# Performance work log

Hardware: AMD Instinct MI355X
Metric: run time of the kernel (lower is better)

The kernel has to match this reference:

```python
import jax, jax.numpy as jnp
import numpy as np

NEG = jnp.float32(-1e30)  # finite stand-in for -inf (keeps grads NaN-free)

B, S = 8, 256


def _inside_logZ(scores, mask):
    """CYK inside algorithm. scores/mask: [B, S, S]. Returns scalar logZ.

    Recurrence (widths w = 1..S-1, processed as a scan over anti-diagonals):
      s[i, i+1] = scores[i, i+1]
      s[i, i+w] = scores[i, i+w] + logsumexp_{k=i+1..i+w-1} (s[i, k] + s[k, i+w])
    logZ = sum_b s[b, 0, lens[b]].
    """
    Bsz, Sl, _ = scores.shape
    lens = mask[:, 0].sum(-1)                    # [B] sentence lengths
    idx = jnp.arange(Sl)
    rows = idx[:, None]                          # [S,1] span start i
    m = idx[None, :]                             # [1,S] split offset (k = i+m)
    km = jnp.clip(rows + m, 0, Sl - 1)           # [S,S] split index k, clipped reads

    def step(s, w):
        # s: [B,S,S] chart. Process all spans of width w at once.
        j = jnp.clip(rows + w, 0, Sl - 1)        # [S,1] span end (clipped)
        left = s[:, rows, km]                    # s[b, i, i+m]      -> [B,S,S]
        right = s[:, km, j]                      # s[b, i+m, i+w]    -> [B,S,S]
        valid = (m >= 1) & (m <= w - 1) & (rows + w < Sl)
        lse = jax.nn.logsumexp(jnp.where(valid, left + right, NEG), axis=-1)  # [B,S]
        diag = scores[:, idx, jnp.clip(idx + w, 0, Sl - 1)]                    # [B,S]
        val = diag + jnp.where(w == 1, 0.0, lse)
        # scatter onto the w-th diagonal; out-of-range (i+w >= S) lanes dropped
        s = s.at[:, idx, idx + w].set(val, mode='drop')
        return s, None

    s0 = jnp.full((Bsz, Sl, Sl), NEG, scores.dtype)
    s, _ = jax.lax.scan(step, s0, jnp.arange(1, Sl))
    return s[jnp.arange(Bsz), 0, lens].sum()


def setup_inputs() -> dict:
    key = jax.random.key(0)
    scores = jax.random.normal(key, (B, S, S), dtype=jnp.float32)
    # strict upper-triangular mask (all sentences full length S-1 tokens)
    mask = jnp.triu(jnp.ones((S, S), dtype=bool), k=1)
    mask = jnp.broadcast_to(mask, (B, S, S))
    return {"scores": scores, "mask": mask}


def reference(scores, mask):
    # forward(scores, mask, target=None, mbr=True): marginals = d logZ / d scores
    marginals = jax.grad(lambda sc: _inside_logZ(sc, mask))(scores)
    return marginals
```

## Files before the change

kernel.cpp:

```cpp
#include <hip/hip_runtime.h>

#define SL 256
#define BATCH 8
#define NT 1024
#define W0 16
#define LDSF 33152
#define TABN 264
#define LDSB ((LDSF + 32 + TABN + 3 * 256) * 4)

__device__ __forceinline__ int rowOff(int j) {
  int jp = (j > 128) ? (256 - j) : j;
  int base = (jp - 1) * 260;
  if (j > 128) base += (jp + 3) & ~3;
  return base;
}

template <int G>
__device__ __forceinline__ float grpSum(float v) {
#pragma unroll
  for (int o = G >> 1; o; o >>= 1) v += __shfl_xor(v, o, 64);
  return v;
}

__device__ __forceinline__ void barrier_lgkm() {
  __builtin_amdgcn_sched_barrier(0);
  asm volatile("s_waitcnt lgkmcnt(0)" ::: "memory");
  __builtin_amdgcn_s_barrier();
  __builtin_amdgcn_sched_barrier(0);
}

__device__ void rescaleE(int tid, float dc, int wcur, float* sh,
                         float* Es1, float* Es2, float* Es3,
                         const int* __restrict__ tab) {
  const int lane = tid & 63, wave = tid >> 6;
  for (int j = 1 + wave; j < SL; j += 16) {
    int jlo = j - wcur; if (jlo < 0) jlo = 0;
    int base = tab[j];
    for (int i = jlo + lane; i < j; i += 64)
      sh[base + i] *= __expf(-dc * (float)(j - i));
  }
  const float f1 = __expf(-dc);
  const float f2 = f1 * f1;
  const float f3 = f2 * f1;
  for (int x = tid; x < SL; x += NT) {
    Es1[x] *= f1; Es2[x] *= f2; Es3[x] *= f3;
  }
}

template <int G>
__device__ void insideP(int wlo, int whi, int t0, int tid,
                        const float* __restrict__ sc, float* __restrict__ sh,
                        float* __restrict__ red, const int* __restrict__ tab,
                        float* __restrict__ Es1, float* __restrict__ Es2,
                        float* __restrict__ Es3) {
  constexpr int LG = (G == 4) ? 2 : (G == 8) ? 3 : (G == 16) ? 4 : 5;
  constexpr int NG = 64 / G;
  const int lane = tid & 63, wv = tid >> 6;
  const int l = lane >> LG, lig = lane & (G - 1);
  const int i = wv * (NG - 1) + l;
  for (int w = wlo; w <= whi; w += 2) {
    const int t = t0 + ((w - wlo) >> 1);
    const float fl = red[16 + ((t - 1) & 1)];
    const unsigned wm1 = (unsigned)(w - 1);
    const unsigned wm2 = (unsigned)(w - 2);
    const bool vw = i < SL - w;
    const bool vw1 = (l < NG - 1) && (i < SL - w - 1);
    const int jw = (i + w < SL) ? i + w : SL - 1;
    const int jw1 = (i + w + 1 < SL) ? i + w + 1 : SL - 1;
    const int ojw = tab[jw], ojw1 = tab[jw1];
    const float scw = sc[i * SL + jw];
    const float scw1 = sc[i * SL + jw1];
    float a0 = 0.f, a1 = 0.f, b0 = 0.f, b1 = 0.f;
    if (vw) {
      for (int s4 = ((i + 1) & ~3) + 4 * lig; s4 < i + w; s4 += 4 * G) {
        float4 rw = *(const float4*)(sh + ojw + s4);
        float4 rw1 = *(const float4*)(sh + ojw1 + s4);
        int4 tv = *(const int4*)(tab + s4);
        float e0 = sh[tv.x + i], e1 = sh[tv.y + i];
        float e2 = sh[tv.z + i], e3 = sh[tv.w + i];
        const int d0 = s4 - i;
        float f0 = ((unsigned)(d0 - 1) < wm1) ? e0 : 0.f;
        float f1 = ((unsigned)(d0    ) < wm1) ? e1 : 0.f;
        float f2 = ((unsigned)(d0 + 1) < wm1) ? e2 : 0.f;
        float f3 = ((unsigned)(d0 + 2) < wm1) ? e3 : 0.f;
        a0 = fmaf(f0, rw.x, a0); a1 = fmaf(f1, rw.y, a1);
        a0 = fmaf(f2, rw.z, a0); a1 = fmaf(f3, rw.w, a1);
        float g0 = ((unsigned)(d0 - 2) < wm2) ? e0 : 0.f;
        float g1 = ((unsigned)(d0 - 1) < wm2) ? e1 : 0.f;
        float g2 = ((unsigned)(d0    ) < wm2) ? e2 : 0.f;
        float g3 = ((unsigned)(d0 + 1) < wm2) ? e3 : 0.f;
        b0 = fmaf(g0, rw1.x, b0); b1 = fmaf(g1, rw1.y, b1);
        b0 = fmaf(g2, rw1.z, b0); b1 = fmaf(g3, rw1.w, b1);
      }
    }
    float accw = grpSum<G>(a0 + a1);
    float accw1 = grpSum<G>(b0 + b1);
    float Ew = __expf(scw) * accw;
    if (vw && lig == 0) {
      sh[ojw + i] = Ew;
      if (accw > 3.5e19f || accw < 3e-16f) red[16 + (t & 1)] = fmaxf(accw, 1e-30f);
    }
    float EwN = __shfl_down(Ew, G, 64);
    if (vw1) {
      float tot = accw1 + Es1[i] * EwN + Ew * Es1[jw];
      if (lig == 0) {
        sh[ojw1 + i] = __expf(scw1) * tot;
        if (tot > 3.5e19f || tot < 3e-16f) red[16 + (t & 1)] = fmaxf(tot, 1e-30f);
      }
    }
    __syncthreads();
    if (fl != 0.f) {
      float dc = (__logf(fl) + 8.0f) / (float)(w - 2);
      rescaleE(tid, dc, w + 1, sh, Es1, Es2, Es3, tab);
      __syncthreads();
      if (tid == 0) { red[16] = 0.f; red[17] = 0.f; }
      __syncthreads();
    }
  }
}

template <int G>
__device__ void insideQ(int wlo, int whi, int t0, int tid,
                        const float* __restrict__ sc, float* __restrict__ sh,
                        float* __restrict__ red, const int* __restrict__ tab,
                        float* __restrict__ Es1, float* __restrict__ Es2,
                        float* __restrict__ Es3) {
  constexpr int LG = (G == 4) ? 2 : 3;
  constexpr int NG = 64 / G;
  const int lane = tid & 63, wv = tid >> 6;
  const int l = lane >> LG, lig = lane & (G - 1);
  const int i = wv * (NG - 3) + l;
  for (int w = wlo; w <= whi; w += 4) {
    const int t = t0 + ((w - wlo) >> 2);
    const float fl = red[16 + ((t - 1) & 1)];
    const bool v0 = i < SL - w;
    const bool v1 = i < SL - w - 1;
    const bool v2 = i < SL - w - 2;
    const bool v3 = i < SL - w - 3;
    const int j0 = (i + w < SL) ? i + w : SL - 1;
    const int j1 = (i + w + 1 < SL) ? i + w + 1 : SL - 1;
    const int j2 = (i + w + 2 < SL) ? i + w + 2 : SL - 1;
    const int j3 = (i + w + 3 < SL) ? i + w + 3 : SL - 1;
    const int o0 = tab[j0], o1 = tab[j1], o2 = tab[j2], o3 = tab[j3];
    const int rb = i * SL;
    const float s0 = sc[rb + j0], s1 = sc[rb + j1];
    const float s2 = sc[rb + j2], s3 = sc[rb + j3];
    float a0=0.f,a1=0.f,b0=0.f,b1=0.f,c0=0.f,c1=0.f,e4a=0.f,e4b=0.f;
    if (v0) {
      const unsigned mA = (unsigned)(w - 1);
      const unsigned mB = (unsigned)(w - 2);
      const unsigned mC = (unsigned)(w - 3);
      const unsigned mD = (unsigned)(w - 4);
      for (int s4 = ((i + 1) & ~3) + 4 * lig; s4 < i + w; s4 += 4 * G) {
        float4 r0 = *(const float4*)(sh + o0 + s4);
        float4 r1 = *(const float4*)(sh + o1 + s4);
        float4 r2 = *(const float4*)(sh + o2 + s4);
        float4 r3 = *(const float4*)(sh + o3 + s4);
        int4 tv = *(const int4*)(tab + s4);
        float e0 = sh[tv.x + i], e1 = sh[tv.y + i];
        float e2 = sh[tv.z + i], e3 = sh[tv.w + i];
        const int dd = s4 - i;
        float f0 = ((unsigned)(dd - 1) < mA) ? e0 : 0.f;
        float f1 = ((unsigned)(dd    ) < mA) ? e1 : 0.f;
        float f2 = ((unsigned)(dd + 1) < mA) ? e2 : 0.f;
        float f3 = ((unsigned)(dd + 2) < mA) ? e3 : 0.f;
        a0 = fmaf(f0, r0.x, a0); a1 = fmaf(f1, r0.y, a1);
        a0 = fmaf(f2, r0.z, a0); a1 = fmaf(f3, r0.w, a1);
        float g0 = ((unsigned)(dd - 2) < mB) ? e0 : 0.f;
        float g1 = ((unsigned)(dd - 1) < mB) ? e1 : 0.f;
        float g2 = ((unsigned)(dd    ) < mB) ? e2 : 0.f;
        float g3 = ((unsigned)(dd + 1) < mB) ? e3 : 0.f;
        b0 = fmaf(g0, r1.x, b0); b1 = fmaf(g1, r1.y, b1);
        b0 = fmaf(g2, r1.z, b0); b1 = fmaf(g3, r1.w, b1);
        float h0 = ((unsigned)(dd - 3) < mC) ? e0 : 0.f;
        float h1 = ((unsigned)(dd - 2) < mC) ? e1 : 0.f;
        float h2 = ((unsigned)(dd - 1) < mC) ? e2 : 0.f;
        float h3 = ((unsigned)(dd    ) < mC) ? e3 : 0.f;
        c0 = fmaf(h0, r2.x, c0); c1 = fmaf(h1, r2.y, c1);
        c0 = fmaf(h2, r2.z, c0); c1 = fmaf(h3, r2.w, c1);
        float k0 = ((unsigned)(dd - 4) < mD) ? e0 : 0.f;
        float k1 = ((unsigned)(dd - 3) < mD) ? e1 : 0.f;
        float k2 = ((unsigned)(dd - 2) < mD) ? e2 : 0.f;
        float k3 = ((unsigned)(dd - 1) < mD) ? e3 : 0.f;
        e4a = fmaf(k0, r3.x, e4a); e4b = fmaf(k1, r3.y, e4b);
        e4a = fmaf(k2, r3.z, e4a); e4b = fmaf(k3, r3.w, e4b);
      }
    }
    float A0 = grpSum<G>(a0 + a1);
    float A1 = grpSum<G>(b0 + b1);
    float A2 = grpSum<G>(c0 + c1);
    float A3 = grpSum<G>(e4a + e4b);
    const float es1i = Es1[i], es2i = Es2[i], es3i = Es3[i];
    const float E0 = __expf(s0) * A0;
    const float n10 = __shfl_down(E0, G, 64);
    const float n20 = __shfl_down(E0, 2 * G, 64);
    const float n30 = __shfl_down(E0, 3 * G, 64);
    const float T1 = A1 + es1i * n10 + E0 * Es1[j0];
    const float E1v = __expf(s1) * T1;
    const float n11 = __shfl_down(E1v, G, 64);
    const float n21 = __shfl_down(E1v, 2 * G, 64);
    const float T2 = A2 + es1i * n11 + E1v * Es1[j1] + es2i * n20 + E0 * Es2[j0];
    const float E2v = __expf(s2) * T2;
    const float n12 = __shfl_down(E2v, G, 64);
    const float T3 = A3 + es1i * n12 + E2v * Es1[j2] + es2i * n21 + E1v * Es2[j1]
                        + es3i * n30 + E0 * Es3[j0];
    const float E3v = __expf(s3) * T3;
    if (lig == 0) {
      if (v0)                sh[o0 + i] = E0;
      if (v1 && l <= NG - 2) sh[o1 + i] = E1v;
      if (v2 && l <= NG - 3) sh[o2 + i] = E2v;
      if (v3 && l <= NG - 4) sh[o3 + i] = E3v;
      if (v0 && (A0 > 3.5e19f || A0 < 3e-16f)) red[16 + (t & 1)] = fmaxf(A0, 1e-30f);
      if (v3 && l <= NG - 4 && (T3 > 3.5e19f || T3 < 3e-16f))
        red[16 + (t & 1)] = fmaxf(T3, 1e-30f);
    }
    __syncthreads();
    if (fl != 0.f) {
      float dc = (__logf(fl) + 8.0f) / (float)(w - 3);
      rescaleE(tid, dc, w + 3, sh, Es1, Es2, Es3, tab);
      __syncthreads();
      if (tid == 0) { red[16] = 0.f; red[17] = 0.f; }
      __syncthreads();
    }
  }
}

template <int G>
__device__ void outsideP(int wAhi, int wAlo, int tid, const float* __restrict__ sc,
                         float* __restrict__ gOut, const float* __restrict__ Eg,
                         const float* __restrict__ ETg, float* __restrict__ shH,
                         const int* __restrict__ tab, const float* __restrict__ Es1) {
  constexpr int LG = (G == 4) ? 2 : (G == 8) ? 3 : (G == 16) ? 4 : 5;
  constexpr int NG = 64 / G;
  const int lane = tid & 63, wv = tid >> 6;
  const int l = lane >> LG, lig = lane & (G - 1);
  const int p = wv * (NG - 1) + l;
  for (int wA = wAhi; wA >= wAlo; wA -= 2) {
    const int wB = wA - 1;
    const bool vA = p < SL - wA;
    const bool vB = (l >= 1 || wv == 0) && (p < SL - wB);
    const int qA = p + wA, qB = p + wB;
    const int qAc = (qA < SL) ? qA : SL - 1;
    const int qBc = (qB < SL) ? qB : SL - 1;
    const int oA = tab[qAc], oB = tab[qBc];
    const float scA = sc[p * SL + qAc];
    const float scB = sc[p * SL + qBc];
    float EpA = 0.f, EpB = 0.f;
    if (lig == 0) {
      if (vA) EpA = Eg[p * SL + qA];
      if (vB) EpB = Eg[p * SL + qB];
    }
    float a0 = 0.f, a1 = 0.f, b0 = 0.f, b1 = 0.f;
    if (vA || vB) {
      const float* erA = Eg + (size_t)qAc * SL;
      const float* erB = Eg + (size_t)qBc * SL;
      for (int s4 = ((qA + 1) & ~3) + 4 * lig; s4 < SL; s4 += 4 * G) {
        float4 eA = *(const float4*)(erA + s4);
        float4 eB = *(const float4*)(erB + s4);
        int4 tv = *(const int4*)(tab + s4);
        float h0 = shH[tv.x + p], h1 = shH[tv.y + p];
        float h2 = shH[tv.z + p], h3 = shH[tv.w + p];
        float m0 = (s4 + 0 > qA) ? h0 : 0.f, m1 = (s4 + 1 > qA) ? h1 : 0.f;
        float m2 = (s4 + 2 > qA) ? h2 : 0.f, m3 = (s4 + 3 > qA) ? h3 : 0.f;
        a0 = fmaf(eA.x, m0, a0); a1 = fmaf(eA.y, m1, a1);
        a0 = fmaf(eA.z, m2, a0); a1 = fmaf(eA.w, m3, a1);
        b0 = fmaf(eB.x, m0, b0); b1 = fmaf(eB.y, m1, b1);
        b0 = fmaf(eB.z, m2, b0); b1 = fmaf(eB.w, m3, b1);
      }
      for (int s4 = 4 * lig; s4 < p; s4 += 4 * G) {
        float4 ev = *(const float4*)(ETg + (size_t)p * SL + s4);
        float4 hA = *(const float4*)(shH + oA + s4);
        float4 hB = *(const float4*)(shH + oB + s4);
        a0 = fmaf(ev.x, hA.x, a0); a1 = fmaf(ev.y, hA.y, a1);
        a0 = fmaf(ev.z, hA.z, a0); a1 = fmaf(ev.w, hA.w, a1);
        float n0 = (s4 + 0 < p - 1) ? hB.x : 0.f;
        float n1 = (s4 + 1 < p - 1) ? hB.y : 0.f;
        float n2 = (s4 + 2 < p - 1) ? hB.z : 0.f;
        float n3 = (s4 + 3 < p - 1) ? hB.w : 0.f;
        b0 = fmaf(ev.x, n0, b0); b1 = fmaf(ev.y, n1, b1);
        b0 = fmaf(ev.z, n2, b0); b1 = fmaf(ev.w, n3, b1);
      }
    }
    float accA = grpSum<G>(a0 + a1);
    float accBb = grpSum<G>(b0 + b1);
    float HA = __expf(scA) * accA;
    if (vA && lig == 0) {
      shH[oA + p] = HA;
      gOut[p * SL + qA] = EpA * accA;
    }
    float HAup = __shfl_up(HA, G, 64);
    if (vB) {
      float accB = accBb + (vA ? Es1[qBc] * HA : 0.f)
                         + ((p > 0) ? Es1[p - 1] * HAup : 0.f);
      if (lig == 0) {
        shH[oB + p] = __expf(scB) * accB;
        gOut[p * SL + qB] = EpB * accB;
      }
    }
    barrier_lgkm();
  }
}

template <int G>
__device__ void outsideQ(int wAhi, int wAlo, int tid, const float* __restrict__ sc,
                         float* __restrict__ gOut, const float* __restrict__ Eg,
                         const float* __restrict__ ETg, float* __restrict__ shH,
                         const int* __restrict__ tab, const float* __restrict__ Es1,
                         const float* __restrict__ Es2, const float* __restrict__ Es3) {
  constexpr int LG = (G == 4) ? 2 : 3;
  constexpr int NG = 64 / G;
  const int lane = tid & 63, wv = tid >> 6;
  const int l = lane >> LG, lig = lane & (G - 1);
  const int p = wv * (NG - 3) + l;
  for (int wA = wAhi; wA >= wAlo; wA -= 4) {
    const bool v0 = p < SL - wA;
    const bool v1 = p < SL - wA + 1;
    const bool v2 = p < SL - wA + 2;
    const bool v3 = p < SL - wA + 3;
    const int q0 = p + wA, q1 = q0 - 1, q2 = q0 - 2, q3 = q0 - 3;
    const int qc0 = (q0 < SL) ? q0 : SL - 1;
    const int qc1 = (q1 < SL) ? q1 : SL - 1;
    const int qc2 = (q2 < SL) ? q2 : SL - 1;
    const int qc3 = (q3 < SL) ? q3 : SL - 1;
    const int o0 = tab[qc0], o1 = tab[qc1], o2 = tab[qc2], o3 = tab[qc3];
    const int rb = p * SL;
    const float s0 = sc[rb + qc0], s1 = sc[rb + qc1];
    const float s2 = sc[rb + qc2], s3 = sc[rb + qc3];
    float Ep0 = 0.f, Ep1 = 0.f, Ep2 = 0.f, Ep3 = 0.f;
    if (lig == 0) {
      if (v0) Ep0 = Eg[rb + q0];
      if (v1) Ep1 = Eg[rb + q1];
      if (v2) Ep2 = Eg[rb + q2];
      if (v3) Ep3 = Eg[rb + q3];
    }
    float a0=0.f,a1=0.f,b0=0.f,b1=0.f,c0=0.f,c1=0.f,e4a=0.f,e4b=0.f;
    if (v3) {
      const float* er0 = Eg + (size_t)qc0 * SL;
      const float* er1 = Eg + (size_t)qc1 * SL;
      const float* er2 = Eg + (size_t)qc2 * SL;
      const float* er3 = Eg + (size_t)qc3 * SL;
      for (int s4 = ((q0 + 1) & ~3) + 4 * lig; s4 < SL; s4 += 4 * G) {
        float4 e0v = *(const float4*)(er0 + s4);
        float4 e1v = *(const float4*)(er1 + s4);
        float4 e2v = *(const float4*)(er2 + s4);
        float4 e3v = *(const float4*)(er3 + s4);
        int4 tv = *(const int4*)(tab + s4);
        float h0 = (s4 + 0 > q0) ? shH[tv.x + p] : 0.f;
        float h1 = (s4 + 1 > q0) ? shH[tv.y + p] : 0.f;
        float h2 = (s4 + 2 > q0) ? shH[tv.z + p] : 0.f;
        float h3 = (s4 + 3 > q0) ? shH[tv.w + p] : 0.f;
        a0 = fmaf(e0v.x, h0, a0); a1 = fmaf(e0v.y, h1, a1);
        a0 = fmaf(e0v.z, h2, a0); a1 = fmaf(e0v.w, h3, a1);
        b0 = fmaf(e1v.x, h0, b0); b1 = fmaf(e1v.y, h1, b1);
        b0 = fmaf(e1v.z, h2, b0); b1 = fmaf(e1v.w, h3, b1);
        c0 = fmaf(e2v.x, h0, c0); c1 = fmaf(e2v.y, h1, c1);
        c0 = fmaf(e2v.z, h2, c0); c1 = fmaf(e2v.w, h3, c1);
        e4a = fmaf(e3v.x, h0, e4a); e4b = fmaf(e3v.y, h1, e4b);
        e4a = fmaf(e3v.z, h2, e4a); e4b = fmaf(e3v.w, h3, e4b);
      }
      for (int s4 = 4 * lig; s4 < p; s4 += 4 * G) {
        float4 ev = *(const float4*)(ETg + (size_t)p * SL + s4);
        float4 h0v = *(const float4*)(shH + o0 + s4);
        float4 h1v = *(const float4*)(shH + o1 + s4);
        float4 h2v = *(const float4*)(shH + o2 + s4);
        float4 h3v = *(const float4*)(shH + o3 + s4);
        a0 = fmaf(ev.x, h0v.x, a0); a1 = fmaf(ev.y, h0v.y, a1);
        a0 = fmaf(ev.z, h0v.z, a0); a1 = fmaf(ev.w, h0v.w, a1);
        float n0 = (s4 + 0 < p - 1) ? h1v.x : 0.f;
        float n1 = (s4 + 1 < p - 1) ? h1v.y : 0.f;
        float n2 = (s4 + 2 < p - 1) ? h1v.z : 0.f;
        float n3 = (s4 + 3 < p - 1) ? h1v.w : 0.f;
        b0 = fmaf(ev.x, n0, b0); b1 = fmaf(ev.y, n1, b1);
        b0 = fmaf(ev.z, n2, b0); b1 = fmaf(ev.w, n3, b1);
        float x0 = (s4 + 0 < p - 2) ? h2v.x : 0.f;
        float x1 = (s4 + 1 < p - 2) ? h2v.y : 0.f;
        float x2 = (s4 + 2 < p - 2) ? h2v.z : 0.f;
        float x3 = (s4 + 3 < p - 2) ? h2v.w : 0.f;
        c0 = fmaf(ev.x, x0, c0); c1 = fmaf(ev.y, x1, c1);
        c0 = fmaf(ev.z, x2, c0); c1 = fmaf(ev.w, x3, c1);
        float y0 = (s4 + 0 < p - 3) ? h3v.x : 0.f;
        float y1 = (s4 + 1 < p - 3) ? h3v.y : 0.f;
        float y2 = (s4 + 2 < p - 3) ? h3v.z : 0.f;
        float y3 = (s4 + 3 < p - 3) ? h3v.w : 0.f;
        e4a = fmaf(ev.x, y0, e4a); e4b = fmaf(ev.y, y1, e4b);
        e4a = fmaf(ev.z, y2, e4a); e4b = fmaf(ev.w, y3, e4b);
      }
    }
    float A0 = grpSum<G>(a0 + a1);
    float A1 = grpSum<G>(b0 + b1);
    float A2 = grpSum<G>(c0 + c1);
    float A3 = grpSum<G>(e4a + e4b);
    const float ep1 = (p >= 1) ? Es1[p - 1] : 0.f;
    const float ep2 = (p >= 2) ? Es2[p - 2] : 0.f;
    const float ep3 = (p >= 3) ? Es3[p - 3] : 0.f;
    const float H0 = __expf(s0) * A0;
    const float u10 = __shfl_up(H0, G, 64);
    const float u20 = __shfl_up(H0, 2 * G, 64);
    const float u30 = __shfl_up(H0, 3 * G, 64);
    const float T1 = A1 + (v0 ? Es1[qc1] * H0 : 0.f) + ep1 * u10;
    const float H1 = __expf(s1) * T1;
    const float u11 = __shfl_up(H1, G, 64);
    const float u21 = __shfl_up(H1, 2 * G, 64);
    const float T2 = A2 + (v1 ? Es1[qc2] * H1 : 0.f) + ep1 * u11
                        + (v0 ? Es2[qc2] * H0 : 0.f) + ep2 * u20;
    const float H2 = __expf(s2) * T2;
    const float u12 = __shfl_up(H2, G, 64);
    const float T3 = A3 + (v2 ? Es1[qc3] * H2 : 0.f) + ep1 * u12
                        + (v1 ? Es2[qc3] * H1 : 0.f) + ep2 * u21
                        + (v0 ? Es3[qc3] * H0 : 0.f) + ep3 * u30;
    const float H3 = __expf(s3) * T3;
    const bool okl1 = (l >= 1) || (wv == 0);
    const bool okl2 = (l >= 2) || (wv == 0);
    const bool okl3 = (l >= 3) || (wv == 0);
    if (lig == 0) {
      if (v0)         { shH[o0 + p] = H0; gOut[rb + q0] = Ep0 * A0; }
      if (v1 && okl1) { shH[o1 + p] = H1; gOut[rb + q1] = Ep1 * T1; }
      if (v2 && okl2) { shH[o2 + p] = H2; gOut[rb + q2] = Ep2 * T2; }
      if (v3 && okl3) { shH[o3 + p] = H3; gOut[rb + q3] = Ep3 * T3; }
    }
    barrier_lgkm();
  }
}

template <int G>
__device__ void outsideB(int w0, int w1, int tid,
    const float* __restrict__ sc, float* __restrict__ gOut,
    const float* __restrict__ Eg, const float* __restrict__ ETg,
    float* __restrict__ shH, const int* __restrict__ tab) {
  constexpr int LG = (G == 4) ? 2 : (G == 8) ? 3 : (G == 16) ? 4 : (G == 32) ? 5 : 6;
  const int c = tid >> LG, lig = tid & (G - 1);
  for (int w = w0; w >= w1; --w) {
    if (c < SL - w) {
      const int p = c, q = p + w;
      float scv = 0.f, Epq = 0.f;
      if (lig == 0) { scv = sc[p * SL + q]; Epq = Eg[p * SL + q]; }
      float a0 = 0.f, a1 = 0.f;
      const float* er = Eg + (size_t)q * SL;
      for (int s4 = ((q + 1) & ~3) + 4 * lig; s4 < SL; s4 += 4 * G) {
        float4 ev = *(const float4*)(er + s4);
        int4 tv = *(const int4*)(tab + s4);
        float h0 = shH[tv.x + p], h1 = shH[tv.y + p];
        float h2 = shH[tv.z + p], h3 = shH[tv.w + p];
        a0 = fmaf(ev.x, (s4 + 0 > q) ? h0 : 0.f, a0);
        a1 = fmaf(ev.y, (s4 + 1 > q) ? h1 : 0.f, a1);
        a0 = fmaf(ev.z, (s4 + 2 > q) ? h2 : 0.f, a0);
        a1 = fmaf(ev.w, (s4 + 3 > q) ? h3 : 0.f, a1);
      }
      if (p > 0) {
        const float* et = ETg + (size_t)p * SL;
        const float* hq = shH + tab[q];
        for (int s4 = 4 * lig; s4 < p; s4 += 4 * G) {
          float4 ev = *(const float4*)(et + s4);
          float4 hv = *(const float4*)(hq + s4);
          a0 = fmaf(ev.x, hv.x, a0);
          a1 = fmaf(ev.y, hv.y, a1);
          a0 = fmaf(ev.z, hv.z, a0);
          a1 = fmaf(ev.w, hv.w, a1);
        }
      }
      float acc = grpSum<G>(a0 + a1);
      if (lig == 0) {
        gOut[p * SL + q] = Epq * acc;
        shH[tab[q] + p] = acc * __expf(scv);
      }
    }
    barrier_lgkm();
  }
}

__global__ __launch_bounds__(NT) void cyk_quad(
    const float* __restrict__ scores, float* __restrict__ out,
    float* __restrict__ ws) {
  extern __shared__ float sh[];
  float* red = sh + LDSF;
  int* tab = (int*)(sh + LDSF + 32);
  float* Es1 = sh + LDSF + 32 + TABN;
  float* Es2 = Es1 + 256;
  float* Es3 = Es2 + 256;
  const int b = blockIdx.x;
  const int tid = threadIdx.x;
  const int lane = tid & 63;
  const int wave = tid >> 6;
  const size_t P = (size_t)SL * SL;
  const float* sc = scores + (size_t)b * P;
  float* g   = out + (size_t)b * P;
  float* Eg  = ws + (size_t)b * P;
  float* ETg = ws + (size_t)(BATCH + b) * P;

  for (int idx = tid * 4; idx < LDSF; idx += NT * 4)
    *(float4*)(sh + idx) = make_float4(0.f, 0.f, 0.f, 0.f);
  if (tid < 32) red[tid] = 0.f;
  if (tid < TABN) tab[tid] = (tid >= 1 && tid <= 255) ? rowOff(tid) : 0;
  if (tid < 256) { Es1[tid] = 0.f; Es2[tid] = 0.f; Es3[tid] = 0.f; }
  __syncthreads();

  for (int i = tid; i < SL - 1; i += NT)
    sh[tab[i + 1] + i] = sc[i * SL + i + 1];
  __syncthreads();

  {
    const int c4 = tid >> 2, lig = tid & 3;
    for (int w = 2; w <= W0; ++w) {
      if (c4 < SL - w) {
        const int i = c4, j = i + w;
        const int oj = tab[j];
        float scv = 0.f;
        if (lig == 0) scv = sc[i * SL + j];
        float m = -1e30f, sum = 0.f;
        for (int k = i + 1 + lig; k < j; k += 4) {
          float t = sh[tab[k] + i] + sh[oj + k];
          float nm = fmaxf(m, t);
          sum = sum * __expf(m - nm) + __expf(t - nm);
          m = nm;
        }
#pragma unroll
        for (int o = 2; o; o >>= 1) {
          float mo = __shfl_xor(m, o, 64);
          float so = __shfl_xor(sum, o, 64);
          float nm = fmaxf(m, mo);
          sum = sum * __expf(m - nm) + so * __expf(mo - nm);
          m = nm;
        }
        if (lig == 0) sh[oj + i] = scv + m + __logf(sum);
      }
      __syncthreads();
    }
  }

  {
    int idx = tid < SL - W0 ? tid : SL - W0 - 1;
    float v = sh[tab[idx + W0] + idx];
#pragma unroll
    for (int o = 32; o; o >>= 1) v = fmaxf(v, __shfl_xor(v, o, 64));
    if (lane == 0) red[wave] = v;
  }
  __syncthreads();
  float cc;
  {
    float mx = red[0];
#pragma unroll
    for (int t = 1; t < 16; ++t) mx = fmaxf(mx, red[t]);
    cc = mx / (float)W0;
  }

  for (int w = 1; w <= W0; ++w) {
    for (int i = tid; i < SL - w; i += NT) {
      int o = tab[i + w] + i;
      float E = __expf(sh[o] - cc * (float)w);
      sh[o] = E;
      if (w == 1) Es1[i] = E;
      if (w == 2) Es2[i] = E;
      if (w == 3) Es3[i] = E;
    }
  }
  if (tid == 0) { red[16] = 0.f; red[17] = 0.f; }
  __syncthreads();

  insideP<4>(17, 43, 1, tid, sc, sh, red, tab, Es1, Es2, Es3);
  insideQ<4>(45, 169, 15, tid, sc, sh, red, tab, Es1, Es2, Es3);
  insideQ<8>(173, 249, 47, tid, sc, sh, red, tab, Es1, Es2, Es3);
  insideP<32>(253, 253, 67, tid, sc, sh, red, tab, Es1, Es2, Es3);

  {
    float acc = 0.f;
    if (wave == 0) {
      const int o255 = tab[255];
      for (int k = 1 + lane; k < 255; k += 64)
        acc += sh[tab[k]] * sh[o255 + k];
#pragma unroll
      for (int o = 32; o; o >>= 1) acc += __shfl_xor(acc, o, 64);
      if (lane == 0) sh[o255] = __expf(sc[SL - 1]) * acc;
    }
    __syncthreads();
  }

  for (int idx = tid; idx < SL * SL; idx += NT) {
    int j = idx >> 8, i = idx & 255;
    if (i < j) ETg[idx] = sh[tab[j] + i];
  }
  for (int idx = tid; idx < SL * SL; idx += NT) {
    int i = idx >> 8, k = idx & 255;
    if (k > i) Eg[idx] = sh[tab[k] + i];
  }
  if (tid == 0) {
    float Er = sh[tab[SL - 1]];
    red[20] = (Er > 0.f) ? __expf(sc[SL - 1]) / Er : 0.f;
    g[SL - 1] = 1.0f;
  }
  __syncthreads();

  for (int idx = tid * 4; idx < LDSF; idx += NT * 4)
    *(float4*)(sh + idx) = make_float4(0.f, 0.f, 0.f, 0.f);
  __syncthreads();
  if (tid == 0) sh[tab[SL - 1]] = red[20];
  __syncthreads();

  outsideP<32>(254, 254, tid, sc, g, Eg, ETg, sh, tab, Es1);
  outsideQ<8>(252, 176, tid, sc, g, Eg, ETg, sh, tab, Es1, Es2, Es3);
  outsideQ<4>(172, 48, tid, sc, g, Eg, ETg, sh, tab, Es1, Es2, Es3);
  outsideP<4>(44, 18, tid, sc, g, Eg, ETg, sh, tab, Es1);
  outsideB<4>(16, 1, tid, sc, g, Eg, ETg, sh, tab);
}

__device__ __forceinline__ float grpMaxR(float v, int G) {
#pragma unroll
  for (int o = 32; o; o >>= 1)
    if (o < G) v = fmaxf(v, __shfl_xor(v, o, 64));
  return v;
}
__device__ __forceinline__ float grpSumR(float v, int G) {
#pragma unroll
  for (int o = 32; o; o >>= 1)
    if (o < G) v += __shfl_xor(v, o, 64);
  return v;
}

__global__ __launch_bounds__(NT) void cyk_io_fb(
    const float* __restrict__ scores, float* __restrict__ out,
    float* __restrict__ ws) {
  const int b = blockIdx.x;
  const int tid = threadIdx.x;
  const size_t P = (size_t)SL * SL;
  const float* sc = scores + (size_t)b * P;
  float* g = out + (size_t)b * P;
  float* s = ws + (size_t)b * P;
  float* l = ws + (size_t)(BATCH + b) * P;

  for (int i = tid; i < SL - 1; i += NT) {
    s[i * SL + i + 1] = sc[i * SL + i + 1];
    l[i * SL + i + 1] = 0.f;
  }
  __syncthreads();

  for (int w = 2; w < SL; ++w) {
    const int cells = SL - w;
    int G = NT / cells;
    G = (G >= 64) ? 64 : (1 << (31 - __clz(G)));
    const int lg = 31 - __clz(G);
    const int c = tid >> lg;
    const int lig = tid & (G - 1);
    if (c < cells) {
      const int i = c, j = i + w;
      const float* srow = s + i * SL;
      float m = -INFINITY;
      for (int k = i + 1 + lig; k < j; k += G)
        m = fmaxf(m, srow[k] + s[k * SL + j]);
      m = grpMaxR(m, G);
      float sum = 0.f;
      for (int k = i + 1 + lig; k < j; k += G)
        sum += __expf(srow[k] + s[k * SL + j] - m);
      sum = grpSumR(sum, G);
      if (lig == 0) {
        const float lse = m + __logf(sum);
        s[i * SL + j] = sc[i * SL + j] + lse;
        l[i * SL + j] = lse;
      }
    }
    __syncthreads();
  }

  if (tid == 0) g[0 * SL + (SL - 1)] = 1.0f;
  __syncthreads();

  for (int w = SL - 2; w >= 1; --w) {
    const int cells = SL - w;
    int G = NT / cells;
    G = (G >= 64) ? 64 : (1 << (31 - __clz(G)));
    const int lg = 31 - __clz(G);
    const int c = tid >> lg;
    const int lig = tid & (G - 1);
    if (c < cells) {
      const int p = c, q = p + w;
      const float spq = s[p * SL + q];
      const int TR = SL - 1 - q;
      const int T = TR + p;
      float acc = 0.f;
      for (int t = lig; t < T; t += G) {
        if (t < TR) {
          const int j = q + 1 + t;
          acc += g[p * SL + j] * __expf(spq + s[q * SL + j] - l[p * SL + j]);
        } else {
          const int i = t - TR;
          acc += g[i * SL + q] * __expf(s[i * SL + p] + spq - l[i * SL + q]);
        }
      }
      acc = grpSumR(acc, G);
      if (lig == 0) g[p * SL + q] = acc;
    }
    __syncthreads();
  }
}

extern "C" void kernel_launch(void* const* d_in, const int* in_sizes, int n_in,
                              void* d_out, int out_size, void* d_ws, size_t ws_size,
                              hipStream_t stream) {
  const float* scores = (const float*)d_in[0];
  float* out = (float*)d_out;
  float* ws = (float*)d_ws;

  const size_t sq = (size_t)SL * SL * sizeof(float);
  hipMemsetAsync(d_out, 0, (size_t)BATCH * sq, stream);

  int dev = 0;
  hipGetDevice(&dev);
  int maxShm = 0;
  hipDeviceGetAttribute(&maxShm, hipDeviceAttributeMaxSharedMemoryPerBlock, dev);
  (void)hipFuncSetAttribute(reinterpret_cast<const void*>(cyk_quad),
                            hipFuncAttributeMaxDynamicSharedMemorySize, LDSB);

  if (maxShm >= LDSB && ws_size >= (size_t)2 * BATCH * sq) {
    hipMemsetAsync(ws, 0, (size_t)2 * BATCH * sq, stream);
    cyk_quad<<<BATCH, NT, LDSB, stream>>>(scores, out, ws);
  } else {
    cyk_io_fb<<<BATCH, NT, 0, stream>>>(scores, out, ws);
  }
}
```

Baseline: 653.7 us.

## Mirror inside/outside chart rows in global memory for contiguous float4 operand loads

Each inside and outside value is now also written to a row-major global copy (Eg, plus a new Hg buffer), so the inner split loops read one operand as a contiguous float4 from global memory. This replaces four table-indexed scalar LDS gathers per chunk. The inner loops are also split into an unmasked steady-state body with masked head and tail chunks, and the end-of-inside Eg copy loop is dropped. In exchange, rescaling must now sweep the whole global Eg array, the workspace grows to three buffers that must be zeroed, and the outside barrier changes from barrier_lgkm to __syncthreads so that global writes become visible; each step's operands now depend on global memory latency and coherence within the block.

```diff
diff --git a/kernel.cpp b/kernel.cpp
--- a/kernel.cpp
+++ b/kernel.cpp
@@ -31,7 +31,7 @@
 
 __device__ void rescaleE(int tid, float dc, int wcur, float* sh,
                          float* Es1, float* Es2, float* Es3,
-                         const int* __restrict__ tab) {
+                         const int* __restrict__ tab, float* __restrict__ Eg) {
   const int lane = tid & 63, wave = tid >> 6;
   for (int j = 1 + wave; j < SL; j += 16) {
     int jlo = j - wcur; if (jlo < 0) jlo = 0;
@@ -39,6 +39,11 @@
     for (int i = jlo + lane; i < j; i += 64)
       sh[base + i] *= __expf(-dc * (float)(j - i));
   }
+  for (int idx = tid; idx < SL * SL; idx += NT) {
+    int i2 = idx >> 8, j2 = idx & 255;
+    int wd = j2 - i2;
+    if (wd > 0 && wd <= wcur) Eg[idx] *= __expf(-dc * (float)wd);
+  }
   const float f1 = __expf(-dc);
   const float f2 = f1 * f1;
   const float f3 = f2 * f1;
@@ -52,7 +57,7 @@
                         const float* __restrict__ sc, float* __restrict__ sh,
                         float* __restrict__ red, const int* __restrict__ tab,
                         float* __restrict__ Es1, float* __restrict__ Es2,
-                        float* __restrict__ Es3) {
+                        float* __restrict__ Es3, float* __restrict__ Eg) {
   constexpr int LG = (G == 4) ? 2 : (G == 8) ? 3 : (G == 16) ? 4 : 5;
   constexpr int NG = 64 / G;
   const int lane = tid & 63, wv = tid >> 6;
@@ -98,20 +103,23 @@
     float Ew = __expf(scw) * accw;
     if (vw && lig == 0) {
       sh[ojw + i] = Ew;
+      Eg[i * SL + jw] = Ew;
       if (accw > 3.5e19f || accw < 3e-16f) red[16 + (t & 1)] = fmaxf(accw, 1e-30f);
     }
     float EwN = __shfl_down(Ew, G, 64);
     if (vw1) {
       float tot = accw1 + Es1[i] * EwN + Ew * Es1[jw];
       if (lig == 0) {
-        sh[ojw1 + i] = __expf(scw1) * tot;
+        float E1o = __expf(scw1) * tot;
+        sh[ojw1 + i] = E1o;
+        Eg[i * SL + jw1] = E1o;
         if (tot > 3.5e19f || tot < 3e-16f) red[16 + (t & 1)] = fmaxf(tot, 1e-30f);
       }
     }
     __syncthreads();
     if (fl != 0.f) {
       float dc = (__logf(fl) + 8.0f) / (float)(w - 2);
-      rescaleE(tid, dc, w + 1, sh, Es1, Es2, Es3, tab);
+      rescaleE(tid, dc, w + 1, sh, Es1, Es2, Es3, tab, Eg);
       __syncthreads();
       if (tid == 0) { red[16] = 0.f; red[17] = 0.f; }
       __syncthreads();
@@ -124,9 +132,10 @@
                         const float* __restrict__ sc, float* __restrict__ sh,
                         float* __restrict__ red, const int* __restrict__ tab,
                         float* __restrict__ Es1, float* __restrict__ Es2,
-                        float* __restrict__ Es3) {
+                        float* __restrict__ Es3, float* __restrict__ Eg) {
   constexpr int LG = (G == 4) ? 2 : 3;
   constexpr int NG = 64 / G;
+  constexpr int STR = 4 * G;
   const int lane = tid & 63, wv = tid >> 6;
   const int l = lane >> LG, lig = lane & (G - 1);
   const int i = wv * (NG - 3) + l;
@@ -147,44 +156,62 @@
     const float s2 = sc[rb + j2], s3 = sc[rb + j3];
     float a0=0.f,a1=0.f,b0=0.f,b1=0.f,c0=0.f,c1=0.f,e4a=0.f,e4b=0.f;
     if (v0) {
+      const float* egr = Eg + rb;
+      const int kend = i + w;
       const unsigned mA = (unsigned)(w - 1);
       const unsigned mB = (unsigned)(w - 2);
       const unsigned mC = (unsigned)(w - 3);
       const unsigned mD = (unsigned)(w - 4);
-      for (int s4 = ((i + 1) & ~3) + 4 * lig; s4 < i + w; s4 += 4 * G) {
+      auto mchunk = [&](int s4) {
+        float4 ev = *(const float4*)(egr + s4);
         float4 r0 = *(const float4*)(sh + o0 + s4);
         float4 r1 = *(const float4*)(sh + o1 + s4);
         float4 r2 = *(const float4*)(sh + o2 + s4);
         float4 r3 = *(const float4*)(sh + o3 + s4);
-        int4 tv = *(const int4*)(tab + s4);
-        float e0 = sh[tv.x + i], e1 = sh[tv.y + i];
-        float e2 = sh[tv.z + i], e3 = sh[tv.w + i];
         const int dd = s4 - i;
-        float f0 = ((unsigned)(dd - 1) < mA) ? e0 : 0.f;
-        float f1 = ((unsigned)(dd    ) < mA) ? e1 : 0.f;
-        float f2 = ((unsigned)(dd + 1) < mA) ? e2 : 0.f;
-        float f3 = ((unsigned)(dd + 2) < mA) ? e3 : 0.f;
+        float f0 = ((unsigned)(dd - 1) < mA) ? ev.x : 0.f;
+        float f1 = ((unsigned)(dd    ) < mA) ? ev.y : 0.f;
+        float f2 = ((unsigned)(dd + 1) < mA) ? ev.z : 0.f;
+        float f3 = ((unsigned)(dd + 2) < mA) ? ev.w : 0.f;
         a0 = fmaf(f0, r0.x, a0); a1 = fmaf(f1, r0.y, a1);
         a0 = fmaf(f2, r0.z, a0); a1 = fmaf(f3, r0.w, a1);
-        float g0 = ((unsigned)(dd - 2) < mB) ? e0 : 0.f;
-        float g1 = ((unsigned)(dd - 1) < mB) ? e1 : 0.f;
-        float g2 = ((unsigned)(dd    ) < mB) ? e2 : 0.f;
-        float g3 = ((unsigned)(dd + 1) < mB) ? e3 : 0.f;
+        float g0 = ((unsigned)(dd - 2) < mB) ? ev.x : 0.f;
+        float g1 = ((unsigned)(dd - 1) < mB) ? ev.y : 0.f;
+        float g2 = ((unsigned)(dd    ) < mB) ? ev.z : 0.f;
+        float g3 = ((unsigned)(dd + 1) < mB) ? ev.w : 0.f;
         b0 = fmaf(g0, r1.x, b0); b1 = fmaf(g1, r1.y, b1);
         b0 = fmaf(g2, r1.z, b0); b1 = fmaf(g3, r1.w, b1);
-        float h0 = ((unsigned)(dd - 3) < mC) ? e0 : 0.f;
-        float h1 = ((unsigned)(dd - 2) < mC) ? e1 : 0.f;
-        float h2 = ((unsigned)(dd - 1) < mC) ? e2 : 0.f;
-        float h3 = ((unsigned)(dd    ) < mC) ? e3 : 0.f;
+        float h0 = ((unsigned)(dd - 3) < mC) ? ev.x : 0.f;
+        float h1 = ((unsigned)(dd - 2) < mC) ? ev.y : 0.f;
+        float h2 = ((unsigned)(dd - 1) < mC) ? ev.z : 0.f;
+        float h3 = ((unsigned)(dd    ) < mC) ? ev.w : 0.f;
         c0 = fmaf(h0, r2.x, c0); c1 = fmaf(h1, r2.y, c1);
         c0 = fmaf(h2, r2.z, c0); c1 = fmaf(h3, r2.w, c1);
-        float k0 = ((unsigned)(dd - 4) < mD) ? e0 : 0.f;
-        float k1 = ((unsigned)(dd - 3) < mD) ? e1 : 0.f;
-        float k2 = ((unsigned)(dd - 2) < mD) ? e2 : 0.f;
-        float k3 = ((unsigned)(dd - 1) < mD) ? e3 : 0.f;
+        float k0 = ((unsigned)(dd - 4) < mD) ? ev.x : 0.f;
+        float k1 = ((unsigned)(dd - 3) < mD) ? ev.y : 0.f;
+        float k2 = ((unsigned)(dd - 2) < mD) ? ev.z : 0.f;
+        float k3 = ((unsigned)(dd - 1) < mD) ? ev.w : 0.f;
         e4a = fmaf(k0, r3.x, e4a); e4b = fmaf(k1, r3.y, e4b);
         e4a = fmaf(k2, r3.z, e4a); e4b = fmaf(k3, r3.w, e4b);
-      }
+      };
+      int s4 = ((i + 1) & ~3) + 4 * lig;
+      if (s4 < kend) { mchunk(s4); s4 += STR; }
+      for (; s4 + 4 <= kend; s4 += STR) {
+        float4 ev = *(const float4*)(egr + s4);
+        float4 r0 = *(const float4*)(sh + o0 + s4);
+        float4 r1 = *(const float4*)(sh + o1 + s4);
+        float4 r2 = *(const float4*)(sh + o2 + s4);
+        float4 r3 = *(const float4*)(sh + o3 + s4);
+        a0 = fmaf(ev.x, r0.x, a0); a1 = fmaf(ev.y, r0.y, a1);
+        a0 = fmaf(ev.z, r0.z, a0); a1 = fmaf(ev.w, r0.w, a1);
+        b0 = fmaf(ev.x, r1.x, b0); b1 = fmaf(ev.y, r1.y, b1);
+        b0 = fmaf(ev.z, r1.z, b0); b1 = fmaf(ev.w, r1.w, b1);
+        c0 = fmaf(ev.x, r2.x, c0); c1 = fmaf(ev.y, r2.y, c1);
+        c0 = fmaf(ev.z, r2.z, c0); c1 = fmaf(ev.w, r2.w, c1);
+        e4a = fmaf(ev.x, r3.x, e4a); e4b = fmaf(ev.y, r3.y, e4b);
+        e4a = fmaf(ev.z, r3.z, e4a); e4b = fmaf(ev.w, r3.w, e4b);
+      }
+      for (; s4 < kend; s4 += STR) mchunk(s4);
     }
     float A0 = grpSum<G>(a0 + a1);
     float A1 = grpSum<G>(b0 + b1);
@@ -206,10 +233,10 @@
                         + es3i * n30 + E0 * Es3[j0];
     const float E3v = __expf(s3) * T3;
     if (lig == 0) {
-      if (v0)                sh[o0 + i] = E0;
-      if (v1 && l <= NG - 2) sh[o1 + i] = E1v;
-      if (v2 && l <= NG - 3) sh[o2 + i] = E2v;
-      if (v3 && l <= NG - 4) sh[o3 + i] = E3v;
+      if (v0)                { sh[o0 + i] = E0;  Eg[rb + j0] = E0; }
+      if (v1 && l <= NG - 2) { sh[o1 + i] = E1v; Eg[rb + j1] = E1v; }
+      if (v2 && l <= NG - 3) { sh[o2 + i] = E2v; Eg[rb + j2] = E2v; }
+      if (v3 && l <= NG - 4) { sh[o3 + i] = E3v; Eg[rb + j3] = E3v; }
       if (v0 && (A0 > 3.5e19f || A0 < 3e-16f)) red[16 + (t & 1)] = fmaxf(A0, 1e-30f);
       if (v3 && l <= NG - 4 && (T3 > 3.5e19f || T3 < 3e-16f))
         red[16 + (t & 1)] = fmaxf(T3, 1e-30f);
@@ -217,7 +244,7 @@
     __syncthreads();
     if (fl != 0.f) {
       float dc = (__logf(fl) + 8.0f) / (float)(w - 3);
-      rescaleE(tid, dc, w + 3, sh, Es1, Es2, Es3, tab);
+      rescaleE(tid, dc, w + 3, sh, Es1, Es2, Es3, tab, Eg);
       __syncthreads();
       if (tid == 0) { red[16] = 0.f; red[17] = 0.f; }
       __syncthreads();
@@ -229,7 +256,8 @@
 __device__ void outsideP(int wAhi, int wAlo, int tid, const float* __restrict__ sc,
                          float* __restrict__ gOut, const float* __restrict__ Eg,
                          const float* __restrict__ ETg, float* __restrict__ shH,
-                         const int* __restrict__ tab, const float* __restrict__ Es1) {
+                         const int* __restrict__ tab, const float* __restrict__ Es1,
+                         float* __restrict__ Hg) {
   constexpr int LG = (G == 4) ? 2 : (G == 8) ? 3 : (G == 16) ? 4 : 5;
   constexpr int NG = 64 / G;
   const int lane = tid & 63, wv = tid >> 6;
@@ -286,6 +314,7 @@
     float HA = __expf(scA) * accA;
     if (vA && lig == 0) {
       shH[oA + p] = HA;
+      Hg[p * SL + qA] = HA;
       gOut[p * SL + qA] = EpA * accA;
     }
     float HAup = __shfl_up(HA, G, 64);
@@ -293,11 +322,13 @@
       float accB = accBb + (vA ? Es1[qBc] * HA : 0.f)
                          + ((p > 0) ? Es1[p - 1] * HAup : 0.f);
       if (lig == 0) {
-        shH[oB + p] = __expf(scB) * accB;
+        float HB = __expf(scB) * accB;
+        shH[oB + p] = HB;
+        Hg[p * SL + qB] = HB;
         gOut[p * SL + qB] = EpB * accB;
       }
     }
-    barrier_lgkm();
+    __syncthreads();
   }
 }
 
@@ -306,9 +337,11 @@
                          float* __restrict__ gOut, const float* __restrict__ Eg,
                          const float* __restrict__ ETg, float* __restrict__ shH,
                          const int* __restrict__ tab, const float* __restrict__ Es1,
-                         const float* __restrict__ Es2, const float* __restrict__ Es3) {
+                         const float* __restrict__ Es2, const float* __restrict__ Es3,
+                         float* __restrict__ Hg) {
   constexpr int LG = (G == 4) ? 2 : 3;
   constexpr int NG = 64 / G;
+  constexpr int STR = 4 * G;
   const int lane = tid & 63, wv = tid >> 6;
   const int l = lane >> LG, lig = lane & (G - 1);
   const int p = wv * (NG - 3) + l;
@@ -335,20 +368,22 @@
     }
     float a0=0.f,a1=0.f,b0=0.f,b1=0.f,c0=0.f,c1=0.f,e4a=0.f,e4b=0.f;
     if (v3) {
+      const float* hgr = Hg + rb;
       const float* er0 = Eg + (size_t)qc0 * SL;
       const float* er1 = Eg + (size_t)qc1 * SL;
       const float* er2 = Eg + (size_t)qc2 * SL;
       const float* er3 = Eg + (size_t)qc3 * SL;
-      for (int s4 = ((q0 + 1) & ~3) + 4 * lig; s4 < SL; s4 += 4 * G) {
+      int s4 = ((q0 + 1) & ~3) + 4 * lig;
+      if (s4 < SL) {
+        float4 hv = *(const float4*)(hgr + s4);
         float4 e0v = *(const float4*)(er0 + s4);
         float4 e1v = *(const float4*)(er1 + s4);
         float4 e2v = *(const float4*)(er2 + s4);
         float4 e3v = *(const float4*)(er3 + s4);
-        int4 tv = *(const int4*)(tab + s4);
-        float h0 = (s4 + 0 > q0) ? shH[tv.x + p] : 0.f;
-        float h1 = (s4 + 1 > q0) ? shH[tv.y + p] : 0.f;
-        float h2 = (s4 + 2 > q0) ? shH[tv.z + p] : 0.f;
-        float h3 = (s4 + 3 > q0) ? shH[tv.w + p] : 0.f;
+        float h0 = (s4 + 0 > q0) ? hv.x : 0.f;
+        float h1 = (s4 + 1 > q0) ? hv.y : 0.f;
+        float h2 = (s4 + 2 > q0) ? hv.z : 0.f;
+        float h3 = (s4 + 3 > q0) ? hv.w : 0.f;
         a0 = fmaf(e0v.x, h0, a0); a1 = fmaf(e0v.y, h1, a1);
         a0 = fmaf(e0v.z, h2, a0); a1 = fmaf(e0v.w, h3, a1);
         b0 = fmaf(e1v.x, h0, b0); b1 = fmaf(e1v.y, h1, b1);
@@ -357,31 +392,64 @@
         c0 = fmaf(e2v.z, h2, c0); c1 = fmaf(e2v.w, h3, c1);
         e4a = fmaf(e3v.x, h0, e4a); e4b = fmaf(e3v.y, h1, e4b);
         e4a = fmaf(e3v.z, h2, e4a); e4b = fmaf(e3v.w, h3, e4b);
-      }
-      for (int s4 = 4 * lig; s4 < p; s4 += 4 * G) {
-        float4 ev = *(const float4*)(ETg + (size_t)p * SL + s4);
-        float4 h0v = *(const float4*)(shH + o0 + s4);
-        float4 h1v = *(const float4*)(shH + o1 + s4);
-        float4 h2v = *(const float4*)(shH + o2 + s4);
-        float4 h3v = *(const float4*)(shH + o3 + s4);
+        s4 += STR;
+      }
+      for (; s4 < SL; s4 += STR) {
+        float4 hv = *(const float4*)(hgr + s4);
+        float4 e0v = *(const float4*)(er0 + s4);
+        float4 e1v = *(const float4*)(er1 + s4);
+        float4 e2v = *(const float4*)(er2 + s4);
+        float4 e3v = *(const float4*)(er3 + s4);
+        a0 = fmaf(e0v.x, hv.x, a0); a1 = fmaf(e0v.y, hv.y, a1);
+        a0 = fmaf(e0v.z, hv.z, a0); a1 = fmaf(e0v.w, hv.w, a1);
+        b0 = fmaf(e1v.x, hv.x, b0); b1 = fmaf(e1v.y, hv.y, b1);
+        b0 = fmaf(e1v.z, hv.z, b0); b1 = fmaf(e1v.w, hv.w, b1);
+        c0 = fmaf(e2v.x, hv.x, c0); c1 = fmaf(e2v.y, hv.y, c1);
+        c0 = fmaf(e2v.z, hv.z, c0); c1 = fmaf(e2v.w, hv.w, c1);
+        e4a = fmaf(e3v.x, hv.x, e4a); e4b = fmaf(e3v.y, hv.y, e4b);
+        e4a = fmaf(e3v.z, hv.z, e4a); e4b = fmaf(e3v.w, hv.w, e4b);
+      }
+      const float* etr = ETg + (size_t)p * SL;
+      int s5 = 4 * lig;
+      for (; s5 + 4 <= p - 3; s5 += STR) {
+        float4 ev = *(const float4*)(etr + s5);
+        float4 h0v = *(const float4*)(shH + o0 + s5);
+        float4 h1v = *(const float4*)(shH + o1 + s5);
+        float4 h2v = *(const float4*)(shH + o2 + s5);
+        float4 h3v = *(const float4*)(shH + o3 + s5);
         a0 = fmaf(ev.x, h0v.x, a0); a1 = fmaf(ev.y, h0v.y, a1);
         a0 = fmaf(ev.z, h0v.z, a0); a1 = fmaf(ev.w, h0v.w, a1);
-        float n0 = (s4 + 0 < p - 1) ? h1v.x : 0.f;
-        float n1 = (s4 + 1 < p - 1) ? h1v.y : 0.f;
-        float n2 = (s4 + 2 < p - 1) ? h1v.z : 0.f;
-        float n3 = (s4 + 3 < p - 1) ? h1v.w : 0.f;
+        b0 = fmaf(ev.x, h1v.x, b0); b1 = fmaf(ev.y, h1v.y, b1);
+        b0 = fmaf(ev.z, h1v.z, b0); b1 = fmaf(ev.w, h1v.w, b1);
+        c0 = fmaf(ev.x, h2v.x, c0); c1 = fmaf(ev.y, h2v.y, c1);
+        c0 = fmaf(ev.z, h2v.z, c0); c1 = fmaf(ev.w, h2v.w, c1);
+        e4a = fmaf(ev.x, h3v.x, e4a); e4b = fmaf(ev.y, h3v.y, e4b);
+        e4a = fmaf(ev.z, h3v.z, e4a); e4b = fmaf(ev.w, h3v.w, e4b);
+      }
+      for (; s5 < p; s5 += STR) {
+        float4 ev = *(const float4*)(etr + s5);
+        float4 h0v = *(const float4*)(shH + o0 + s5);
+        float4 h1v = *(const float4*)(shH + o1 + s5);
+        float4 h2v = *(const float4*)(shH + o2 + s5);
+        float4 h3v = *(const float4*)(shH + o3 + s5);
+        a0 = fmaf(ev.x, h0v.x, a0); a1 = fmaf(ev.y, h0v.y, a1);
+        a0 = fmaf(ev.z, h0v.z, a0); a1 = fmaf(ev.w, h0v.w, a1);
+        float n0 = (s5 + 0 < p - 1) ? h1v.x : 0.f;
+        float n1 = (s5 + 1 < p - 1) ? h1v.y : 0.f;
+        float n2 = (s5 + 2 < p - 1) ? h1v.z : 0.f;
+        float n3 = (s5 + 3 < p - 1) ? h1v.w : 0.f;
         b0 = fmaf(ev.x, n0, b0); b1 = fmaf(ev.y, n1, b1);
         b0 = fmaf(ev.z, n2, b0); b1 = fmaf(ev.w, n3, b1);
-        float x0 = (s4 + 0 < p - 2) ? h2v.x : 0.f;
-        float x1 = (s4 + 1 < p - 2) ? h2v.y : 0.f;
-        float x2 = (s4 + 2 < p - 2) ? h2v.z : 0.f;
-        float x3 = (s4 + 3 < p - 2) ? h2v.w : 0.f;
+        float x0 = (s5 + 0 < p - 2) ? h2v.x : 0.f;
+        float x1 = (s5 + 1 < p - 2) ? h2v.y : 0.f;
+        float x2 = (s5 + 2 < p - 2) ? h2v.z : 0.f;
+        float x3 = (s5 + 3 < p - 2) ? h2v.w : 0.f;
         c0 = fmaf(ev.x, x0, c0); c1 = fmaf(ev.y, x1, c1);
         c0 = fmaf(ev.z, x2, c0); c1 = fmaf(ev.w, x3, c1);
-        float y0 = (s4 + 0 < p - 3) ? h3v.x : 0.f;
-        float y1 = (s4 + 1 < p - 3) ? h3v.y : 0.f;
-        float y2 = (s4 + 2 < p - 3) ? h3v.z : 0.f;
-        float y3 = (s4 + 3 < p - 3) ? h3v.w : 0.f;
+        float y0 = (s5 + 0 < p - 3) ? h3v.x : 0.f;
+        float y1 = (s5 + 1 < p - 3) ? h3v.y : 0.f;
+        float y2 = (s5 + 2 < p - 3) ? h3v.z : 0.f;
+        float y3 = (s5 + 3 < p - 3) ? h3v.w : 0.f;
         e4a = fmaf(ev.x, y0, e4a); e4b = fmaf(ev.y, y1, e4b);
         e4a = fmaf(ev.z, y2, e4a); e4b = fmaf(ev.w, y3, e4b);
       }
@@ -413,12 +481,12 @@
     const bool okl2 = (l >= 2) || (wv == 0);
     const bool okl3 = (l >= 3) || (wv == 0);
     if (lig == 0) {
-      if (v0)         { shH[o0 + p] = H0; gOut[rb + q0] = Ep0 * A0; }
-      if (v1 && okl1) { shH[o1 + p] = H1; gOut[rb + q1] = Ep1 * T1; }
-      if (v2 && okl2) { shH[o2 + p] = H2; gOut[rb + q2] = Ep2 * T2; }
-      if (v3 && okl3) { shH[o3 + p] = H3; gOut[rb + q3] = Ep3 * T3; }
-    }
-    barrier_lgkm();
+      if (v0)         { shH[o0 + p] = H0; Hg[rb + q0] = H0; gOut[rb + q0] = Ep0 * A0; }
+      if (v1 && okl1) { shH[o1 + p] = H1; Hg[rb + q1] = H1; gOut[rb + q1] = Ep1 * T1; }
+      if (v2 && okl2) { shH[o2 + p] = H2; Hg[rb + q2] = H2; gOut[rb + q2] = Ep2 * T2; }
+      if (v3 && okl3) { shH[o3 + p] = H3; Hg[rb + q3] = H3; gOut[rb + q3] = Ep3 * T3; }
+    }
+    __syncthreads();
   }
 }
 
@@ -486,6 +554,7 @@
   float* g   = out + (size_t)b * P;
   float* Eg  = ws + (size_t)b * P;
   float* ETg = ws + (size_t)(BATCH + b) * P;
+  float* Hg  = ws + (size_t)(2 * BATCH + b) * P;
 
   for (int idx = tid * 4; idx < LDSF; idx += NT * 4)
     *(float4*)(sh + idx) = make_float4(0.f, 0.f, 0.f, 0.f);
@@ -548,6 +617,7 @@
       int o = tab[i + w] + i;
       float E = __expf(sh[o] - cc * (float)w);
       sh[o] = E;
+      Eg[i * SL + (i + w)] = E;
       if (w == 1) Es1[i] = E;
       if (w == 2) Es2[i] = E;
       if (w == 3) Es3[i] = E;
@@ -556,10 +626,10 @@
   if (tid == 0) { red[16] = 0.f; red[17] = 0.f; }
   __syncthreads();
 
-  insideP<4>(17, 43, 1, tid, sc, sh, red, tab, Es1, Es2, Es3);
-  insideQ<4>(45, 169, 15, tid, sc, sh, red, tab, Es1, Es2, Es3);
-  insideQ<8>(173, 249, 47, tid, sc, sh, red, tab, Es1, Es2, Es3);
-  insideP<32>(253, 253, 67, tid, sc, sh, red, tab, Es1, Es2, Es3);
+  insideP<4>(17, 43, 1, tid, sc, sh, red, tab, Es1, Es2, Es3, Eg);
+  insideQ<4>(45, 169, 15, tid, sc, sh, red, tab, Es1, Es2, Es3, Eg);
+  insideQ<8>(173, 249, 47, tid, sc, sh, red, tab, Es1, Es2, Es3, Eg);
+  insideP<32>(253, 253, 67, tid, sc, sh, red, tab, Es1, Es2, Es3, Eg);
 
   {
     float acc = 0.f;
@@ -569,7 +639,11 @@
         acc += sh[tab[k]] * sh[o255 + k];
 #pragma unroll
       for (int o = 32; o; o >>= 1) acc += __shfl_xor(acc, o, 64);
-      if (lane == 0) sh[o255] = __expf(sc[SL - 1]) * acc;
+      if (lane == 0) {
+        float Er = __expf(sc[SL - 1]) * acc;
+        sh[o255] = Er;
+        Eg[SL - 1] = Er;
+      }
     }
     __syncthreads();
   }
@@ -577,10 +651,6 @@
   for (int idx = tid; idx < SL * SL; idx += NT) {
     int j = idx >> 8, i = idx & 255;
     if (i < j) ETg[idx] = sh[tab[j] + i];
-  }
-  for (int idx = tid; idx < SL * SL; idx += NT) {
-    int i = idx >> 8, k = idx & 255;
-    if (k > i) Eg[idx] = sh[tab[k] + i];
   }
   if (tid == 0) {
     float Er = sh[tab[SL - 1]];
@@ -592,13 +662,13 @@
   for (int idx = tid * 4; idx < LDSF; idx += NT * 4)
     *(float4*)(sh + idx) = make_float4(0.f, 0.f, 0.f, 0.f);
   __syncthreads();
-  if (tid == 0) sh[tab[SL - 1]] = red[20];
-  __syncthreads();
-
-  outsideP<32>(254, 254, tid, sc, g, Eg, ETg, sh, tab, Es1);
-  outsideQ<8>(252, 176, tid, sc, g, Eg, ETg, sh, tab, Es1, Es2, Es3);
-  outsideQ<4>(172, 48, tid, sc, g, Eg, ETg, sh, tab, Es1, Es2, Es3);
-  outsideP<4>(44, 18, tid, sc, g, Eg, ETg, sh, tab, Es1);
+  if (tid == 0) { sh[tab[SL - 1]] = red[20]; Hg[SL - 1] = red[20]; }
+  __syncthreads();
+
+  outsideP<32>(254, 254, tid, sc, g, Eg, ETg, sh, tab, Es1, Hg);
+  outsideQ<8>(252, 176, tid, sc, g, Eg, ETg, sh, tab, Es1, Es2, Es3, Hg);
+  outsideQ<4>(172, 48, tid, sc, g, Eg, ETg, sh, tab, Es1, Es2, Es3, Hg);
+  outsideP<4>(44, 18, tid, sc, g, Eg, ETg, sh, tab, Es1, Hg);
   outsideB<4>(16, 1, tid, sc, g, Eg, ETg, sh, tab);
 }
 
@@ -708,8 +778,8 @@
   (void)hipFuncSetAttribute(reinterpret_cast<const void*>(cyk_quad),
                             hipFuncAttributeMaxDynamicSharedMemorySize, LDSB);
 
-  if (maxShm >= LDSB && ws_size >= (size_t)2 * BATCH * sq) {
-    hipMemsetAsync(ws, 0, (size_t)2 * BATCH * sq, stream);
+  if (maxShm >= LDSB && ws_size >= (size_t)3 * BATCH * sq) {
+    hipMemsetAsync(ws, 0, (size_t)3 * BATCH * sq, stream);
     cyk_quad<<<BATCH, NT, LDSB, stream>>>(scores, out, ws);
   } else {
     cyk_io_fb<<<BATCH, NT, 0, stream>>>(scores, out, ws);
```

Measured after the change: 687.4 us. +5.2%, slower.
